# Kernel tuning notes

Measured on AMD Instinct MI355X. Metric: run time of the kernel, lower is better.

Reference implementation:

```python
import jax, jax.numpy as jnp
import numpy as np

# DualAttention dims
D_MODEL = 1024
H_SA = 8          # self-attention heads
H_RA = 8          # relational-attention heads
TOTAL_H = H_SA + H_RA
HEAD_DIM = D_MODEL // TOTAL_H   # 64
KEY_DIM = HEAD_DIM              # 64
N_REL = 8
REL_PROJ = HEAD_DIM * H_RA // N_REL  # 64
B, S = 2, 2048


def apply_rope(x, cos, sin):
    # x: [b, s, h, d]; cos/sin: [s, d//2]. Pairs are (0,1),(2,3),... as in
    # llama-style apply_rotary_emb (reshape(..., -1, 2).unbind(-1)).
    xr, xi = x[..., 0::2], x[..., 1::2]
    c = cos[None, :, None, :]
    s_ = sin[None, :, None, :]
    out = jnp.stack([xr * c - xi * s_, xr * s_ + xi * c], axis=-1)
    return out.reshape(x.shape)


def setup_inputs() -> dict:
    key = jax.random.key(0)
    ks = jax.random.split(key, 16)
    def w(k, shape):
        return jax.random.normal(k, shape, jnp.float32) * 0.02
    x = jax.random.normal(ks[0], (B, S, D_MODEL), jnp.float32)
    symbols = jax.random.normal(ks[1], (B, S, D_MODEL), jnp.float32)
    # real RoPE tables
    pos = np.arange(S, dtype=np.float32)[:, None]
    inv = 1.0 / (10000.0 ** (np.arange(0, KEY_DIM, 2, dtype=np.float32) / KEY_DIM))
    ang = pos * inv[None, :]
    freqs_cos = jnp.asarray(np.cos(ang), jnp.float32)
    freqs_sin = jnp.asarray(np.sin(ang), jnp.float32)
    return dict(
        x=x, symbols=symbols, freqs_cos=freqs_cos, freqs_sin=freqs_sin,
        # self-attention branch (torch Linear weights: [out, in])
        wq_sa=w(ks[2], (H_SA * KEY_DIM, D_MODEL)),
        wk_sa=w(ks[3], (H_SA * KEY_DIM, D_MODEL)),
        wv_sa=w(ks[4], (H_SA * HEAD_DIM, D_MODEL)),
        wo_sa=w(ks[5], (H_SA * HEAD_DIM, H_SA * HEAD_DIM)),
        # relational-attention branch
        wq_attn=w(ks[6], (H_RA * KEY_DIM, D_MODEL)),
        wk_attn=w(ks[7], (H_RA * KEY_DIM, D_MODEL)),
        wq_rel=w(ks[8], (N_REL * REL_PROJ, D_MODEL)),
        wk_rel=w(ks[9], (N_REL * REL_PROJ, D_MODEL)),
        wr=w(ks[10], (H_RA, HEAD_DIM, N_REL)),
        wv_ra=w(ks[11], (H_RA * HEAD_DIM, D_MODEL)),
        wo_ra=w(ks[12], (H_RA * HEAD_DIM, H_RA * HEAD_DIM)),
    )


def reference(x, symbols, freqs_cos, freqs_sin,
              wq_sa, wk_sa, wv_sa, wo_sa,
              wq_attn, wk_attn, wq_rel, wk_rel, wr, wv_ra, wo_ra):
    b, s, _ = x.shape
    attn_scale = 1.0 / np.sqrt(HEAD_DIM).astype(np.float32)
    rel_scale = 1.0 / np.sqrt(REL_PROJ).astype(np.float32)
    causal = jnp.tril(jnp.ones((s, s), dtype=bool))
    neg = jnp.finfo(x.dtype).min

    def heads(t, h, d):
        return t.reshape(b, s, h, d)

    # ---- self-attention branch (causal SDPA with RoPE) ----
    q = apply_rope(heads(x @ wq_sa.T, H_SA, KEY_DIM), freqs_cos, freqs_sin)
    k = apply_rope(heads(x @ wk_sa.T, H_SA, KEY_DIM), freqs_cos, freqs_sin)
    v = heads(x @ wv_sa.T, H_SA, HEAD_DIM)
    scores = jnp.einsum('bihd,bjhd->bhij', q, k) * attn_scale
    a = jax.nn.softmax(jnp.where(causal, scores, neg), axis=-1)
    sa_out = jnp.einsum('bhij,bjhd->bihd', a, v).reshape(b, s, H_SA * HEAD_DIM) @ wo_sa.T

    # ---- relational-attention branch ----
    # attention scores (softmax selection), with RoPE
    qa = apply_rope(heads(x @ wq_attn.T, H_RA, KEY_DIM), freqs_cos, freqs_sin)
    ka = apply_rope(heads(x @ wk_attn.T, H_RA, KEY_DIM), freqs_cos, freqs_sin)
    ra_scores = jnp.einsum('bihd,bjhd->bhij', qa, ka) * attn_scale
    alpha = jax.nn.softmax(jnp.where(causal, ra_scores, neg), axis=-1)
    # relations r(x_i, x_j) in R^{N_REL} (identity rel_activation)
    qr = heads(x @ wq_rel.T, N_REL, REL_PROJ)
    kr = heads(x @ wk_rel.T, N_REL, REL_PROJ)
    rel = jnp.einsum('birp,bjrp->brij', qr, kr) * rel_scale  # [b, R, i, j]
    # symbol values: wv applied to retrieved symbols
    sv = heads(symbols @ wv_ra.T, H_RA, HEAD_DIM)
    attended_sym = jnp.einsum('bhij,bjhd->bihd', alpha, sv)          # [b, i, h, d]
    attended_rel = jnp.einsum('bhij,brij->bihr', alpha, rel)         # [b, i, h, R]
    rel_out = jnp.einsum('bihr,hdr->bihd', attended_rel, wr)
    ra_out = (attended_sym + rel_out).reshape(b, s, H_RA * HEAD_DIM) @ wo_ra.T

    # DualAttention: concat branch outputs along feature dim -> [b, s, d_model]
    return jnp.concatenate([sa_out, ra_out], axis=-1)
```

## Files before the change

kernel.cpp:

```cpp
#include <hip/hip_runtime.h>

#define B_   2
#define S_   2048
#define H_   8
#define D_   64
#define DM_  1024
#define PJ_  512
#define NT_  32
#define NTRI 528
#define NCHK 80

typedef short bf16x8 __attribute__((ext_vector_type(8)));
typedef float f32x4 __attribute__((ext_vector_type(4)));

__device__ __forceinline__ float bf2f(unsigned int u) {
  return __uint_as_float(u << 16);
}
__device__ __forceinline__ unsigned short f2bf(float f) {
  unsigned int u = __float_as_uint(f);
  u += 0x7fffu + ((u >> 16) & 1u);
  return (unsigned short)(u >> 16);
}

__device__ __forceinline__ void glds16(const unsigned short* g, unsigned short* l) {
  __builtin_amdgcn_global_load_lds(
      (const __attribute__((address_space(1))) void*)g,
      (__attribute__((address_space(3))) void*)l, 16, 0, 0);
}

struct CvtJobs {
  const float*    src[12];
  unsigned short* dst[12];
  int             n4[12];
};

__global__ __launch_bounds__(256) void cvt_many(CvtJobs J) {
  const int j = blockIdx.y;
  const int i = blockIdx.x * 256 + threadIdx.x;
  if (i >= J.n4[j]) return;
  const float4 v = ((const float4*)J.src[j])[i];
  ushort4 o;
  o.x = f2bf(v.x); o.y = f2bf(v.y); o.z = f2bf(v.z); o.w = f2bf(v.w);
  ((ushort4*)J.dst[j])[i] = o;
}

__device__ __forceinline__
void gemm128_glds(const unsigned short* __restrict__ A, int m0,
                  const unsigned short* __restrict__ Wb,
                  unsigned short* __restrict__ Cb, int ldc, int KD,
                  unsigned short* As, unsigned short* Bs)
{
  const int tid = threadIdx.x;
  const int wv = tid >> 6, lane = tid & 63;
  const int r15 = lane & 15, quad = lane >> 4;
  const int wm = (wv >> 1) * 64, wn = (wv & 1) * 64;
  f32x4 acc[4][4];
#pragma unroll
  for (int i = 0; i < 4; ++i)
#pragma unroll
    for (int j = 0; j < 4; ++j) acc[i][j] = (f32x4){0.f, 0.f, 0.f, 0.f};

  const int srow = wv * 16 + (lane >> 2);
  const int scol = ((lane & 3) ^ ((lane >> 3) & 3)) * 8;
  const unsigned short* gaA0 = A + (size_t)(m0 + srow) * KD + scol;
  const unsigned short* gaA1 = gaA0 + (size_t)64 * KD;
  const unsigned short* gaB0 = Wb + (size_t)srow * KD + scol;
  const unsigned short* gaB1 = gaB0 + (size_t)64 * KD;
  unsigned short* ldsA0 = As + wv * 512;
  unsigned short* ldsA1 = As + 2048 + wv * 512;
  unsigned short* ldsB0 = Bs + wv * 512;
  unsigned short* ldsB1 = Bs + 2048 + wv * 512;
  const int rxor = (r15 >> 1) & 3;

  for (int kk = 0; kk < KD; kk += 32) {
    __syncthreads();
    glds16(gaA0 + kk, ldsA0);
    glds16(gaA1 + kk, ldsA1);
    glds16(gaB0 + kk, ldsB0);
    glds16(gaB1 + kk, ldsB1);
    __syncthreads();
    bf16x8 af[4], bf[4];
#pragma unroll
    for (int i = 0; i < 4; ++i)
      af[i] = *(const bf16x8*)(As + (wm + i * 16 + r15) * 32 + ((quad ^ rxor) << 3));
#pragma unroll
    for (int j = 0; j < 4; ++j)
      bf[j] = *(const bf16x8*)(Bs + (wn + j * 16 + r15) * 32 + ((quad ^ rxor) << 3));
#pragma unroll
    for (int i = 0; i < 4; ++i)
#pragma unroll
      for (int j = 0; j < 4; ++j)
        acc[i][j] = __builtin_amdgcn_mfma_f32_16x16x32_bf16(af[i], bf[j], acc[i][j], 0, 0, 0);
  }
#pragma unroll
  for (int i = 0; i < 4; ++i)
#pragma unroll
    for (int r = 0; r < 4; ++r) {
      unsigned short* cp = Cb + (size_t)(wm + i * 16 + quad * 4 + r) * ldc + wn + r15;
#pragma unroll
      for (int j = 0; j < 4; ++j) cp[j * 16] = f2bf(acc[i][j][r]);
    }
}

__global__ __launch_bounds__(256)
void proj_tiled(const unsigned short* __restrict__ XB,
                const unsigned short* __restrict__ SYB,
                const unsigned short* __restrict__ Wcat,
                unsigned short* __restrict__ Qbase,
                unsigned short* __restrict__ SV)
{
  __shared__ unsigned short As[128 * 32];
  __shared__ unsigned short Bs[128 * 32];
  const int m0 = blockIdx.x * 128;
  const int ny = blockIdx.y;
  const size_t NB = (size_t)B_ * S_ * PJ_;
  const unsigned short* A;
  const unsigned short* Wb;
  unsigned short* Cb;
  if (ny < 28) {
    const int n0 = ny * 128;
    A  = XB;
    Wb = Wcat + (size_t)n0 * DM_;
    Cb = Qbase + (size_t)(n0 >> 9) * NB + (size_t)m0 * PJ_ + (n0 & 511);
  } else {
    const int n0 = (ny - 28) * 128;
    A  = SYB;
    Wb = Wcat + (size_t)7 * PJ_ * DM_ + (size_t)n0 * DM_;
    Cb = SV + (size_t)m0 * PJ_ + n0;
  }
  gemm128_glds(A, m0, Wb, Cb, PJ_, DM_, As, Bs);
}

__global__ __launch_bounds__(256)
void out_tiled(const unsigned short* __restrict__ Asa,
               const unsigned short* __restrict__ Ara,
               const unsigned short* __restrict__ WOSA,
               const unsigned short* __restrict__ WORA,
               float* __restrict__ Out)
{
  __shared__ unsigned short As[128 * 40];
  __shared__ unsigned short Bs[64 * 40];
  const int m0 = blockIdx.x * 128;
  const int ny = blockIdx.y;
  const int n0 = (ny & 7) * 64;
  const unsigned short* A  = (ny < 8) ? Asa : Ara;
  const unsigned short* Wb = ((ny < 8) ? WOSA : WORA) + (size_t)n0 * PJ_;
  float* Cb = Out + (size_t)m0 * DM_ + ((ny < 8) ? 0 : 512) + n0;

  const int tid = threadIdx.x;
  const int wv = tid >> 6, lane = tid & 63;
  const int r15 = lane & 15, quad = lane >> 4;
  const int wm = wv * 32;
  f32x4 acc[2][4];
#pragma unroll
  for (int i = 0; i < 2; ++i)
#pragma unroll
    for (int j = 0; j < 4; ++j) acc[i][j] = (f32x4){0.f, 0.f, 0.f, 0.f};

  const int arow = tid >> 1, ac = (tid & 1) * 16;
  const int brow = tid >> 2, bc = (tid & 3) * 8;
  const unsigned short* ga = A + (size_t)(m0 + arow) * PJ_ + ac;
  const unsigned short* gb = Wb + (size_t)brow * PJ_ + bc;
  unsigned short* la = As + arow * 40 + ac;
  unsigned short* lb = Bs + brow * 40 + bc;

  for (int kk = 0; kk < PJ_; kk += 32) {
    __syncthreads();
    const uint4 a0 = *(const uint4*)(ga + kk);
    const uint4 a1 = *(const uint4*)(ga + kk + 8);
    const uint4 b0 = *(const uint4*)(gb + kk);
    *(uint4*)la       = a0;
    *(uint4*)(la + 8) = a1;
    *(uint4*)lb       = b0;
    __syncthreads();
    bf16x8 af[2], bf[4];
#pragma unroll
    for (int i = 0; i < 2; ++i)
      af[i] = *(const bf16x8*)(As + (wm + i * 16 + r15) * 40 + quad * 8);
#pragma unroll
    for (int j = 0; j < 4; ++j)
      bf[j] = *(const bf16x8*)(Bs + (j * 16 + r15) * 40 + quad * 8);
#pragma unroll
    for (int i = 0; i < 2; ++i)
#pragma unroll
      for (int j = 0; j < 4; ++j)
        acc[i][j] = __builtin_amdgcn_mfma_f32_16x16x32_bf16(af[i], bf[j], acc[i][j], 0, 0, 0);
  }
#pragma unroll
  for (int i = 0; i < 2; ++i)
#pragma unroll
    for (int r = 0; r < 4; ++r) {
      float* cp = Cb + (size_t)(wm + i * 16 + quad * 4 + r) * DM_ + r15;
#pragma unroll
      for (int j = 0; j < 4; ++j) cp[j * 16] = acc[i][j][r];
    }
}

__global__ __launch_bounds__(256)
void rel_gemm(const unsigned short* __restrict__ QRg, const unsigned short* __restrict__ KRg,
              unsigned short* __restrict__ RelCF)
{
  __shared__ unsigned short As[128 * 72];
  __shared__ unsigned short Bs[128 * 72];
  const int t = blockIdx.x;
  int I = 0;
  while ((I + 1) * (I + 2) / 2 <= t) ++I;
  const int J = t - I * (I + 1) / 2;
  const int rr = blockIdx.y & 7, b = blockIdx.y >> 3;
  const int tid = threadIdx.x;
  const int wv = tid >> 6, lane = tid & 63;
  const int r15 = lane & 15, quad = lane >> 4;

  const int srow = tid >> 1, c32 = (tid & 1) * 32;
  const unsigned short* ga = QRg + (size_t)(b * S_ + I * 128 + srow) * PJ_ + rr * 64 + c32;
  const unsigned short* gb = KRg + (size_t)(b * S_ + J * 128 + srow) * PJ_ + rr * 64 + c32;
  unsigned short* la = As + srow * 72 + c32;
  unsigned short* lb = Bs + srow * 72 + c32;
#pragma unroll
  for (int q = 0; q < 4; ++q) {
    *(uint4*)(la + q * 8) = *(const uint4*)(ga + q * 8);
    *(uint4*)(lb + q * 8) = *(const uint4*)(gb + q * 8);
  }
  __syncthreads();

  const int wm = (wv >> 1) * 64, wn = (wv & 1) * 64;
  const int it64 = 2 * I + (wv >> 1), jt64 = 2 * J + (wv & 1);
  if (jt64 > it64) return;
  f32x4 acc[4][4];
#pragma unroll
  for (int i = 0; i < 4; ++i)
#pragma unroll
    for (int j = 0; j < 4; ++j) acc[i][j] = (f32x4){0.f, 0.f, 0.f, 0.f};
#pragma unroll
  for (int k0 = 0; k0 < 2; ++k0) {
    bf16x8 af[4], bf[4];
#pragma unroll
    for (int i = 0; i < 4; ++i)
      af[i] = *(const bf16x8*)(As + (wm + i * 16 + r15) * 72 + quad * 8 + k0 * 32);
#pragma unroll
    for (int j = 0; j < 4; ++j)
      bf[j] = *(const bf16x8*)(Bs + (wn + j * 16 + r15) * 72 + quad * 8 + k0 * 32);
#pragma unroll
    for (int i = 0; i < 4; ++i)
#pragma unroll
      for (int j = 0; j < 4; ++j)
        acc[i][j] = __builtin_amdgcn_mfma_f32_16x16x32_bf16(af[i], bf[j], acc[i][j], 0, 0, 0);
  }
  unsigned short* out = RelCF + ((size_t)(b * 8 + rr) * NTRI + (size_t)it64 * (it64 + 1) / 2 + jt64) * 4096;
#pragma unroll
  for (int i = 0; i < 4; ++i) {
    unsigned short tmp[16];
#pragma unroll
    for (int j = 0; j < 4; ++j)
#pragma unroll
      for (int r = 0; r < 4; ++r)
        tmp[j * 4 + r] = f2bf(acc[i][j][r] * 0.125f);
    unsigned short* op = out + (size_t)(i * 64 + lane) * 16;
    *(uint4*)op       = *(const uint4*)tmp;
    *(uint4*)(op + 8) = *(const uint4*)(tmp + 8);
  }
}

__global__ __launch_bounds__(256)
void rope_kernel(unsigned short* Q, unsigned short* K,
                 unsigned short* QA, unsigned short* KA,
                 const float* __restrict__ fc,
                 const float* __restrict__ fs) {
  const int idx = blockIdx.x * 256 + threadIdx.x;
  const int t  = idx >> 20;
  const int r  = idx & 0xFFFFF;
  const int ci = r & 31;
  const int h  = (r >> 5) & 7;
  const int s  = (r >> 8) & 2047;
  const int b  = r >> 19;
  unsigned short* P = (t == 0) ? Q : (t == 1) ? K : (t == 2) ? QA : KA;
  const size_t off = ((size_t)(b * S_ + s)) * PJ_ + h * D_ + (ci << 1);
  const float xr = bf2f(P[off]);
  const float xi = bf2f(P[off + 1]);
  const float cs = fc[s * 32 + ci];
  const float sn = fs[s * 32 + ci];
  P[off]     = f2bf(xr * cs - xi * sn);
  P[off + 1] = f2bf(xr * sn + xi * cs);
}

__global__ __launch_bounds__(256)
void flash_part(const unsigned short* __restrict__ Qsa, const unsigned short* __restrict__ Ksa,
                const unsigned short* __restrict__ Vsa,
                const unsigned short* __restrict__ Qra, const unsigned short* __restrict__ Kra,
                const unsigned short* __restrict__ SVra,
                const unsigned short* __restrict__ RelCF,
                unsigned short* __restrict__ PoP, float* __restrict__ lP,
                float* __restrict__ arpP)
{
  __shared__ unsigned short Ks[64][68];
  __shared__ unsigned short Vt[64][68];
  __shared__ unsigned short Ps[64][68];
  const int x = blockIdx.x;
  int it, c;
  if (x < 8)       { it = x;                    c = 0; }
  else if (x < 24) { it = 8 + ((x - 8) >> 1);   c = (x - 8) & 1; }
  else if (x < 48) { it = 16 + (x - 24) / 3;    c = (x - 24) % 3; }
  else             { it = 24 + ((x - 48) >> 2); c = (x - 48) & 3; }
  const int j0 = c * 8;
  const int jend = (j0 + 8 < it + 1) ? (j0 + 8) : (it + 1);
  const bool ra = (blockIdx.y >= 8);
  const int h = blockIdx.y & 7;
  const int b = blockIdx.z;
  const int chunkId = (b * 16 + (int)blockIdx.y) * NCHK + x;
  const unsigned short* Qg = ra ? Qra : Qsa;
  const unsigned short* Kg = ra ? Kra : Ksa;
  const unsigned short* Vg = ra ? SVra : Vsa;
  const int tid = threadIdx.x;
  const int wv = tid >> 6, lane = tid & 63;
  const int r15 = lane & 15, quad = lane >> 4;
  const size_t bh = (size_t)b * S_ * PJ_ + (size_t)h * D_;
  const size_t relStride = (size_t)NTRI * 4096;

  const int kr0 = tid >> 3, kc0 = (tid & 7) << 3;
  const int kr1 = (tid + 256) >> 3;
  const unsigned short* kgp = Kg + bh + kc0;
  const unsigned short* vgp = Vg + bh + (size_t)lane * PJ_ + wv * 8;

  const unsigned short* qp = Qg + bh + (size_t)(it * 64 + wv * 16 + r15) * PJ_ + quad * 8;
  const bf16x8 aq0 = *(const bf16x8*)qp;
  const bf16x8 aq1 = *(const bf16x8*)(qp + 32);

  unsigned short one8[8];
#pragma unroll
  for (int i = 0; i < 8; ++i) one8[i] = 0x3F80;
  const bf16x8 ones = *(const bf16x8*)one8;

  f32x4 o_acc[4];
  f32x4 l_acc = {0.f, 0.f, 0.f, 0.f};
  float arp[4][8];
#pragma unroll
  for (int n = 0; n < 4; ++n) o_acc[n] = (f32x4){0.f, 0.f, 0.f, 0.f};
#pragma unroll
  for (int r = 0; r < 4; ++r)
#pragma unroll
    for (int rr = 0; rr < 8; ++rr) arp[r][rr] = 0.f;
  const int row0 = it * 64 + wv * 16 + quad * 4;
  const size_t relTileBase = (size_t)(b * 8) * NTRI * 4096
                           + (size_t)(it * (it + 1)) / 2 * 4096
                           + (size_t)(wv * 64 + lane) * 16;

  uint4 ka0, ka1, va0, va1;
  {
    const size_t jb = (size_t)j0 * 64 * PJ_;
    ka0 = *(const uint4*)(kgp + jb + (size_t)kr0 * PJ_);
    ka1 = *(const uint4*)(kgp + jb + (size_t)kr1 * PJ_);
    va0 = *(const uint4*)(vgp + jb);
    va1 = *(const uint4*)(vgp + jb + 32);
  }
  {
    *(uint4*)&Ks[kr0][kc0] = ka0;
    *(uint4*)&Ks[kr1][kc0] = ka1;
    unsigned short t8[8];
    *(uint4*)t8 = va0;
#pragma unroll
    for (int m = 0; m < 8; ++m) Vt[wv * 8 + m][lane] = t8[m];
    *(uint4*)t8 = va1;
#pragma unroll
    for (int m = 0; m < 8; ++m) Vt[wv * 8 + 32 + m][lane] = t8[m];
  }
  __syncthreads();

  for (int jt = j0; jt < jend; ++jt) {
    const bool more = (jt + 1 < jend);
    if (more) {
      const size_t jb = (size_t)(jt + 1) * 64 * PJ_;
      ka0 = *(const uint4*)(kgp + jb + (size_t)kr0 * PJ_);
      ka1 = *(const uint4*)(kgp + jb + (size_t)kr1 * PJ_);
      va0 = *(const uint4*)(vgp + jb);
      va1 = *(const uint4*)(vgp + jb + 32);
    }
    uint4 pre[8];
    const unsigned short* rtBase = RelCF + relTileBase + (size_t)jt * 4096;
    if (ra) {
      const unsigned short* rt = rtBase;
#pragma unroll
      for (int q = 0; q < 4; ++q) {
        pre[2 * q]     = *(const uint4*)rt;
        pre[2 * q + 1] = *(const uint4*)(rt + 8);
        rt += relStride;
      }
    }
    f32x4 s[4];
#pragma unroll
    for (int n = 0; n < 4; ++n) s[n] = (f32x4){0.f, 0.f, 0.f, 0.f};
#pragma unroll
    for (int k0 = 0; k0 < 2; ++k0) {
      const bf16x8 af = k0 ? aq1 : aq0;
#pragma unroll
      for (int n = 0; n < 4; ++n) {
        const bf16x8 bf = *(const bf16x8*)&Ks[n * 16 + r15][quad * 8 + k0 * 32];
        s[n] = __builtin_amdgcn_mfma_f32_16x16x32_bf16(af, bf, s[n], 0, 0, 0);
      }
    }
    if (jt == it) {
#pragma unroll
      for (int n = 0; n < 4; ++n)
#pragma unroll
        for (int r = 0; r < 4; ++r) {
          const bool ok = (jt * 64 + n * 16 + r15 <= row0 + r);
          s[n][r] = ok ? __expf(s[n][r] * 0.125f - 4.0f) : 0.f;
        }
    } else {
#pragma unroll
      for (int n = 0; n < 4; ++n)
#pragma unroll
        for (int r = 0; r < 4; ++r)
          s[n][r] = __expf(s[n][r] * 0.125f - 4.0f);
    }
#pragma unroll
    for (int n = 0; n < 4; ++n)
#pragma unroll
      for (int r = 0; r < 4; ++r)
        Ps[wv * 16 + quad * 4 + r][n * 16 + r15] = f2bf(s[n][r]);
    if (ra) {
      const unsigned short* rt2 = rtBase + 4 * relStride;
#pragma unroll
      for (int rr = 0; rr < 8; ++rr) {
        unsigned short rv[16];
        if (rr < 4) {
          *(uint4*)rv       = pre[2 * rr];
          *(uint4*)(rv + 8) = pre[2 * rr + 1];
        } else {
          *(uint4*)rv       = *(const uint4*)rt2;
          *(uint4*)(rv + 8) = *(const uint4*)(rt2 + 8);
          rt2 += relStride;
        }
#pragma unroll
        for (int n = 0; n < 4; ++n)
#pragma unroll
          for (int r = 0; r < 4; ++r)
            arp[r][rr] += s[n][r] * bf2f(rv[n * 4 + r]);
      }
    }
#pragma unroll
    for (int k0 = 0; k0 < 2; ++k0) {
      const bf16x8 pf = *(const bf16x8*)&Ps[wv * 16 + r15][quad * 8 + k0 * 32];
#pragma unroll
      for (int n = 0; n < 4; ++n) {
        const bf16x8 vf = *(const bf16x8*)&Vt[n * 16 + r15][quad * 8 + k0 * 32];
        o_acc[n] = __builtin_amdgcn_mfma_f32_16x16x32_bf16(pf, vf, o_acc[n], 0, 0, 0);
      }
      l_acc = __builtin_amdgcn_mfma_f32_16x16x32_bf16(pf, ones, l_acc, 0, 0, 0);
    }
    if (more) {
      __syncthreads();
      *(uint4*)&Ks[kr0][kc0] = ka0;
      *(uint4*)&Ks[kr1][kc0] = ka1;
      unsigned short t8[8];
      *(uint4*)t8 = va0;
#pragma unroll
      for (int m = 0; m < 8; ++m) Vt[wv * 8 + m][lane] = t8[m];
      *(uint4*)t8 = va1;
#pragma unroll
      for (int m = 0; m < 8; ++m) Vt[wv * 8 + 32 + m][lane] = t8[m];
      __syncthreads();
    }
  }
  unsigned short* po = PoP + (size_t)chunkId * 4096;
#pragma unroll
  for (int n = 0; n < 4; ++n)
#pragma unroll
    for (int r = 0; r < 4; ++r)
      po[(wv * 16 + quad * 4 + r) * 64 + n * 16 + r15] = f2bf(o_acc[n][r]);
  if (r15 == 0) {
#pragma unroll
    for (int r = 0; r < 4; ++r)
      lP[(size_t)chunkId * 64 + wv * 16 + quad * 4 + r] = l_acc[r];
  }
  if (ra) {
#pragma unroll
    for (int r = 0; r < 4; ++r)
#pragma unroll
      for (int rr = 0; rr < 8; ++rr)
#pragma unroll
        for (int o = 1; o < 16; o <<= 1)
          arp[r][rr] += __shfl_xor(arp[r][rr], o);
    if (r15 == 0) {
#pragma unroll
      for (int r = 0; r < 4; ++r) {
        float* ap = arpP + (size_t)chunkId * 512 + (wv * 16 + quad * 4 + r) * 8;
#pragma unroll
        for (int rr = 0; rr < 8; ++rr) ap[rr] = arp[r][rr];
      }
    }
  }
}

__global__ __launch_bounds__(256)
void flash_merge(const unsigned short* __restrict__ PoP, const float* __restrict__ lP,
                 const float* __restrict__ arpP, const float* __restrict__ wrF,
                 unsigned short* __restrict__ Osa, unsigned short* __restrict__ Ora)
{
  const int it = blockIdx.x;
  const int hh = blockIdx.y;
  const int b  = blockIdx.z;
  const bool ra = (hh >= 8);
  const int h = hh & 7;
  const int nc = it / 8 + 1;
  int cb;
  if (it < 8)       cb = it;
  else if (it < 16) cb = 8 + 2 * (it - 8);
  else if (it < 24) cb = 24 + 3 * (it - 16);
  else              cb = 48 + 4 * (it - 24);
  const int cid0 = (b * 16 + hh) * NCHK + cb;
  const int tid = threadIdx.x;
  const int row = tid >> 2;
  const int cg  = tid & 3;

  float L = 0.f;
  for (int c = 0; c < nc; ++c) L += lP[(size_t)(cid0 + c) * 64 + row];
  const float inv = 1.f / L;

  float o[16];
#pragma unroll
  for (int k = 0; k < 16; ++k) o[k] = 0.f;
  for (int c = 0; c < nc; ++c) {
    const unsigned short* pp = PoP + (size_t)(cid0 + c) * 4096 + row * 64 + cg * 16;
    unsigned short t[16];
    *(uint4*)t       = *(const uint4*)pp;
    *(uint4*)(t + 8) = *(const uint4*)(pp + 8);
#pragma unroll
    for (int k = 0; k < 16; ++k) o[k] += bf2f(t[k]);
  }
  if (ra) {
    float A[8];
#pragma unroll
    for (int rr = 0; rr < 8; ++rr) A[rr] = 0.f;
    for (int c = 0; c < nc; ++c) {
      const float* ap = arpP + (size_t)(cid0 + c) * 512 + row * 8;
#pragma unroll
      for (int rr = 0; rr < 8; ++rr) A[rr] += ap[rr];
    }
#pragma unroll
    for (int k = 0; k < 16; ++k) {
      const float* wp = wrF + ((size_t)h * 64 + cg * 16 + k) * 8;
      float ro = 0.f;
#pragma unroll
      for (int rr = 0; rr < 8; ++rr) ro += A[rr] * wp[rr];
      o[k] += ro;
    }
  }
  const size_t bh = (size_t)b * S_ * PJ_ + (size_t)h * D_;
  unsigned short* op = (ra ? Ora : Osa) + bh + (size_t)(it * 64 + row) * PJ_ + cg * 16;
#pragma unroll
  for (int k = 0; k < 16; ++k) op[k] = f2bf(o[k] * inv);
}

extern "C" void kernel_launch(void* const* d_in, const int* in_sizes, int n_in,
                              void* d_out, int out_size, void* d_ws, size_t ws_size,
                              hipStream_t stream)
{
  (void)in_sizes; (void)n_in; (void)out_size; (void)ws_size;
  const float* x    = (const float*)d_in[0];
  const float* sym  = (const float*)d_in[1];
  const float* fc   = (const float*)d_in[2];
  const float* fs   = (const float*)d_in[3];
  const float* wqsa = (const float*)d_in[4];
  const float* wksa = (const float*)d_in[5];
  const float* wvsa = (const float*)d_in[6];
  const float* wosa = (const float*)d_in[7];
  const float* wqat = (const float*)d_in[8];
  const float* wkat = (const float*)d_in[9];
  const float* wqre = (const float*)d_in[10];
  const float* wkre = (const float*)d_in[11];
  const float* wr   = (const float*)d_in[12];
  const float* wvra = (const float*)d_in[13];
  const float* wora = (const float*)d_in[14];

  unsigned short* wsb = (unsigned short*)d_ws;
  const size_t NX = (size_t)B_ * S_ * DM_;
  const size_t NB = (size_t)B_ * S_ * PJ_;
  const size_t NW = (size_t)PJ_ * DM_;
  const size_t NO = (size_t)PJ_ * PJ_;
  const size_t NR = (size_t)B_ * 8 * NTRI * 4096;
  const size_t NCH = (size_t)B_ * 16 * NCHK;

  size_t off = 0;
  unsigned short* XB   = wsb + off; off += NX;
  unsigned short* SYB  = wsb + off; off += NX;
  unsigned short* WB[8];
  for (int i = 0; i < 8; ++i) { WB[i] = wsb + off; off += NW; }
  unsigned short* WOSA = wsb + off; off += NO;
  unsigned short* WORA = wsb + off; off += NO;
  unsigned short* Q    = wsb + off; off += NB;
  unsigned short* K    = wsb + off; off += NB;
  unsigned short* V    = wsb + off; off += NB;
  unsigned short* QA   = wsb + off; off += NB;
  unsigned short* KA   = wsb + off; off += NB;
  unsigned short* QR   = wsb + off; off += NB;
  unsigned short* KR   = wsb + off; off += NB;
  unsigned short* SV   = wsb + off; off += NB;
  unsigned short* Asa  = wsb + off; off += NB;
  unsigned short* Ara  = wsb + off; off += NB;
  unsigned short* RelCF = wsb + off; off += NR;
  unsigned short* PoP  = XB;
  float* lP   = (float*)(wsb + off); off += NCH * 64 * 2;
  float* arpP = (float*)(wsb + off); off += NCH * 512 * 2;

  CvtJobs cj;
  cj.src[0]  = x;    cj.dst[0]  = XB;    cj.n4[0]  = (int)(NX / 4);
  cj.src[1]  = sym;  cj.dst[1]  = SYB;   cj.n4[1]  = (int)(NX / 4);
  cj.src[2]  = wqsa; cj.dst[2]  = WB[0]; cj.n4[2]  = (int)(NW / 4);
  cj.src[3]  = wksa; cj.dst[3]  = WB[1]; cj.n4[3]  = (int)(NW / 4);
  cj.src[4]  = wvsa; cj.dst[4]  = WB[2]; cj.n4[4]  = (int)(NW / 4);
  cj.src[5]  = wqat; cj.dst[5]  = WB[3]; cj.n4[5]  = (int)(NW / 4);
  cj.src[6]  = wkat; cj.dst[6]  = WB[4]; cj.n4[6]  = (int)(NW / 4);
  cj.src[7]  = wqre; cj.dst[7]  = WB[5]; cj.n4[7]  = (int)(NW / 4);
  cj.src[8]  = wkre; cj.dst[8]  = WB[6]; cj.n4[8]  = (int)(NW / 4);
  cj.src[9]  = wvra; cj.dst[9]  = WB[7]; cj.n4[9]  = (int)(NW / 4);
  cj.src[10] = wosa; cj.dst[10] = WOSA;  cj.n4[10] = (int)(NO / 4);
  cj.src[11] = wora; cj.dst[11] = WORA;  cj.n4[11] = (int)(NO / 4);
  cvt_many<<<dim3(4096, 12), dim3(256), 0, stream>>>(cj);

  proj_tiled<<<dim3(32, 32), dim3(256), 0, stream>>>(XB, SYB, WB[0], Q, SV);
  rope_kernel<<<dim3(16384), dim3(256), 0, stream>>>(Q, K, QA, KA, fc, fs);
  rel_gemm<<<dim3(136, 16), dim3(256), 0, stream>>>(QR, KR, RelCF);
  flash_part<<<dim3(NCHK, 16, B_), dim3(256), 0, stream>>>(
      Q, K, V, QA, KA, SV, RelCF, PoP, lP, arpP);
  flash_merge<<<dim3(NT_, 16, B_), dim3(256), 0, stream>>>(
      PoP, lP, arpP, wr, Asa, Ara);
  out_tiled<<<dim3(32, 16), dim3(256), 0, stream>>>(Asa, Ara, WOSA, WORA, (float*)d_out);
}
```

Before: 332.1 us.

## Pre-transpose V in a separate kernel and read K/V fragments directly from global

```diff
diff --git a/kernel.cpp b/kernel.cpp
--- a/kernel.cpp
+++ b/kernel.cpp
@@ -284,16 +284,42 @@
 }
 
 __global__ __launch_bounds__(256)
+void transpose_v(const unsigned short* __restrict__ V,
+                 const unsigned short* __restrict__ SV,
+                 unsigned short* __restrict__ VtSA,
+                 unsigned short* __restrict__ VtRA)
+{
+  __shared__ unsigned short T[64][72];
+  const int s0 = blockIdx.x * 64;
+  const int d0 = blockIdx.y * 64;
+  const int b  = blockIdx.z & 1;
+  const int rb = blockIdx.z >> 1;
+  const unsigned short* src = (rb ? SV : V) + (size_t)b * S_ * PJ_;
+  unsigned short* dst = (rb ? VtRA : VtSA) + (size_t)b * PJ_ * S_;
+  const int tid = threadIdx.x;
+  const int r = tid >> 3, c8 = (tid & 7) * 8;
+  *(uint4*)&T[r][c8]      = *(const uint4*)(src + (size_t)(s0 + r) * PJ_ + d0 + c8);
+  *(uint4*)&T[r + 32][c8] = *(const uint4*)(src + (size_t)(s0 + r + 32) * PJ_ + d0 + c8);
+  __syncthreads();
+#pragma unroll
+  for (int half = 0; half < 2; ++half) {
+    const int dr = r + half * 32;
+    unsigned short o[8];
+#pragma unroll
+    for (int k = 0; k < 8; ++k) o[k] = T[c8 + k][dr];
+    *(uint4*)(dst + (size_t)(d0 + dr) * S_ + s0 + c8) = *(const uint4*)o;
+  }
+}
+
+__global__ __launch_bounds__(256)
 void flash_part(const unsigned short* __restrict__ Qsa, const unsigned short* __restrict__ Ksa,
-                const unsigned short* __restrict__ Vsa,
+                const unsigned short* __restrict__ Vtsa,
                 const unsigned short* __restrict__ Qra, const unsigned short* __restrict__ Kra,
-                const unsigned short* __restrict__ SVra,
+                const unsigned short* __restrict__ Vtra,
                 const unsigned short* __restrict__ RelCF,
                 unsigned short* __restrict__ PoP, float* __restrict__ lP,
                 float* __restrict__ arpP)
 {
-  __shared__ unsigned short Ks[64][68];
-  __shared__ unsigned short Vt[64][68];
   __shared__ unsigned short Ps[64][68];
   const int x = blockIdx.x;
   int it, c;
@@ -309,17 +335,15 @@
   const int chunkId = (b * 16 + (int)blockIdx.y) * NCHK + x;
   const unsigned short* Qg = ra ? Qra : Qsa;
   const unsigned short* Kg = ra ? Kra : Ksa;
-  const unsigned short* Vg = ra ? SVra : Vsa;
+  const unsigned short* Vt = ra ? Vtra : Vtsa;
   const int tid = threadIdx.x;
   const int wv = tid >> 6, lane = tid & 63;
   const int r15 = lane & 15, quad = lane >> 4;
   const size_t bh = (size_t)b * S_ * PJ_ + (size_t)h * D_;
   const size_t relStride = (size_t)NTRI * 4096;
 
-  const int kr0 = tid >> 3, kc0 = (tid & 7) << 3;
-  const int kr1 = (tid + 256) >> 3;
-  const unsigned short* kgp = Kg + bh + kc0;
-  const unsigned short* vgp = Vg + bh + (size_t)lane * PJ_ + wv * 8;
+  const unsigned short* kfb = Kg + bh + (size_t)r15 * PJ_ + quad * 8;
+  const unsigned short* vfb = Vt + ((size_t)b * PJ_ + h * 64 + r15) * S_ + quad * 8;
 
   const unsigned short* qp = Qg + bh + (size_t)(it * 64 + wv * 16 + r15) * PJ_ + quad * 8;
   const bf16x8 aq0 = *(const bf16x8*)qp;
@@ -344,36 +368,7 @@
                            + (size_t)(it * (it + 1)) / 2 * 4096
                            + (size_t)(wv * 64 + lane) * 16;
 
-  uint4 ka0, ka1, va0, va1;
-  {
-    const size_t jb = (size_t)j0 * 64 * PJ_;
-    ka0 = *(const uint4*)(kgp + jb + (size_t)kr0 * PJ_);
-    ka1 = *(const uint4*)(kgp + jb + (size_t)kr1 * PJ_);
-    va0 = *(const uint4*)(vgp + jb);
-    va1 = *(const uint4*)(vgp + jb + 32);
-  }
-  {
-    *(uint4*)&Ks[kr0][kc0] = ka0;
-    *(uint4*)&Ks[kr1][kc0] = ka1;
-    unsigned short t8[8];
-    *(uint4*)t8 = va0;
-#pragma unroll
-    for (int m = 0; m < 8; ++m) Vt[wv * 8 + m][lane] = t8[m];
-    *(uint4*)t8 = va1;
-#pragma unroll
-    for (int m = 0; m < 8; ++m) Vt[wv * 8 + 32 + m][lane] = t8[m];
-  }
-  __syncthreads();
-
   for (int jt = j0; jt < jend; ++jt) {
-    const bool more = (jt + 1 < jend);
-    if (more) {
-      const size_t jb = (size_t)(jt + 1) * 64 * PJ_;
-      ka0 = *(const uint4*)(kgp + jb + (size_t)kr0 * PJ_);
-      ka1 = *(const uint4*)(kgp + jb + (size_t)kr1 * PJ_);
-      va0 = *(const uint4*)(vgp + jb);
-      va1 = *(const uint4*)(vgp + jb + 32);
-    }
     uint4 pre[8];
     const unsigned short* rtBase = RelCF + relTileBase + (size_t)jt * 4096;
     if (ra) {
@@ -388,14 +383,14 @@
     f32x4 s[4];
 #pragma unroll
     for (int n = 0; n < 4; ++n) s[n] = (f32x4){0.f, 0.f, 0.f, 0.f};
-#pragma unroll
-    for (int k0 = 0; k0 < 2; ++k0) {
-      const bf16x8 af = k0 ? aq1 : aq0;
-#pragma unroll
-      for (int n = 0; n < 4; ++n) {
-        const bf16x8 bf = *(const bf16x8*)&Ks[n * 16 + r15][quad * 8 + k0 * 32];
-        s[n] = __builtin_amdgcn_mfma_f32_16x16x32_bf16(af, bf, s[n], 0, 0, 0);
-      }
+    const unsigned short* kj = kfb + (size_t)(jt * 64) * PJ_;
+#pragma unroll
+    for (int n = 0; n < 4; ++n) {
+      const unsigned short* kp = kj + (size_t)(n * 16) * PJ_;
+      const bf16x8 k0v = *(const bf16x8*)kp;
+      const bf16x8 k1v = *(const bf16x8*)(kp + 32);
+      s[n] = __builtin_amdgcn_mfma_f32_16x16x32_bf16(aq0, k0v, s[n], 0, 0, 0);
+      s[n] = __builtin_amdgcn_mfma_f32_16x16x32_bf16(aq1, k1v, s[n], 0, 0, 0);
     }
     if (jt == it) {
 #pragma unroll
@@ -437,28 +432,16 @@
             arp[r][rr] += s[n][r] * bf2f(rv[n * 4 + r]);
       }
     }
+    const unsigned short* vj = vfb + jt * 64;
 #pragma unroll
     for (int k0 = 0; k0 < 2; ++k0) {
       const bf16x8 pf = *(const bf16x8*)&Ps[wv * 16 + r15][quad * 8 + k0 * 32];
 #pragma unroll
       for (int n = 0; n < 4; ++n) {
-        const bf16x8 vf = *(const bf16x8*)&Vt[n * 16 + r15][quad * 8 + k0 * 32];
+        const bf16x8 vf = *(const bf16x8*)(vj + (size_t)(n * 16) * S_ + k0 * 32);
         o_acc[n] = __builtin_amdgcn_mfma_f32_16x16x32_bf16(pf, vf, o_acc[n], 0, 0, 0);
       }
       l_acc = __builtin_amdgcn_mfma_f32_16x16x32_bf16(pf, ones, l_acc, 0, 0, 0);
-    }
-    if (more) {
-      __syncthreads();
-      *(uint4*)&Ks[kr0][kc0] = ka0;
-      *(uint4*)&Ks[kr1][kc0] = ka1;
-      unsigned short t8[8];
-      *(uint4*)t8 = va0;
-#pragma unroll
-      for (int m = 0; m < 8; ++m) Vt[wv * 8 + m][lane] = t8[m];
-      *(uint4*)t8 = va1;
-#pragma unroll
-      for (int m = 0; m < 8; ++m) Vt[wv * 8 + 32 + m][lane] = t8[m];
-      __syncthreads();
     }
   }
   unsigned short* po = PoP + (size_t)chunkId * 4096;
@@ -601,6 +584,8 @@
   unsigned short* PoP  = XB;
   float* lP   = (float*)(wsb + off); off += NCH * 64 * 2;
   float* arpP = (float*)(wsb + off); off += NCH * 512 * 2;
+  unsigned short* VtSA = wsb + off; off += NB;
+  unsigned short* VtRA = wsb + off; off += NB;
 
   CvtJobs cj;
   cj.src[0]  = x;    cj.dst[0]  = XB;    cj.n4[0]  = (int)(NX / 4);
@@ -619,9 +604,10 @@
 
   proj_tiled<<<dim3(32, 32), dim3(256), 0, stream>>>(XB, SYB, WB[0], Q, SV);
   rope_kernel<<<dim3(16384), dim3(256), 0, stream>>>(Q, K, QA, KA, fc, fs);
+  transpose_v<<<dim3(32, 8, 4), dim3(256), 0, stream>>>(V, SV, VtSA, VtRA);
   rel_gemm<<<dim3(136, 16), dim3(256), 0, stream>>>(QR, KR, RelCF);
   flash_part<<<dim3(NCHK, 16, B_), dim3(256), 0, stream>>>(
-      Q, K, V, QA, KA, SV, RelCF, PoP, lP, arpP);
+      Q, K, VtSA, QA, KA, VtRA, RelCF, PoP, lP, arpP);
   flash_merge<<<dim3(NT_, 16, B_), dim3(256), 0, stream>>>(
       PoP, lP, arpP, wr, Asa, Ara);
   out_tiled<<<dim3(32, 16), dim3(256), 0, stream>>>(Asa, Ara, WOSA, WORA, (float*)d_out);
```

Result: slower. 406.4 us (+22.4%).
